# Performance work log

Measured on AMD Instinct MI355X. Metric: run time of the kernel, lower is better.

Reference implementation:

```python
import jax, jax.numpy as jnp
import numpy as np

N, E, F_IN, DIM, HEADS = 16384, 262144, 128, 64, 4
HID = DIM * HEADS  # 256
NEG = 0.2


def _lin(k, fan_in, fan_out):
    kw, kb = jax.random.split(k)
    s = 1.0 / np.sqrt(fan_in)
    return (jax.random.uniform(kw, (fan_in, fan_out), jnp.float32, -s, s),
            jax.random.uniform(kb, (fan_out,), jnp.float32, -s, s))


def setup_inputs() -> dict:
    key = jax.random.key(0)
    ks = jax.random.split(key, 20)
    x = jax.random.normal(ks[0], (N, F_IN), jnp.float32)
    edge_index = jax.random.randint(ks[1], (2, E), 0, N, jnp.int32)
    Win, b_in = _lin(ks[2], F_IN, DIM)
    Wskip, bskip = _lin(ks[3], DIM, HID)
    # conv1: in=DIM, out per head=DIM, heads=HEADS, concat -> HID
    Wl1, _ = _lin(ks[4], DIM, HID)
    Wr1, _ = _lin(ks[5], DIM, HID)
    att1 = jax.random.normal(ks[6], (HEADS, DIM), jnp.float32) * 0.1
    b1 = jnp.zeros((HID,), jnp.float32)
    # conv2: in=HID, out=HID, heads=1, concat=False
    Wl2, _ = _lin(ks[7], HID, HID)
    Wr2, _ = _lin(ks[8], HID, HID)
    att2 = jax.random.normal(ks[9], (1, HID), jnp.float32) * 0.1
    b2 = jnp.zeros((HID,), jnp.float32)
    # conv3: in=HID, out=HID, heads=1, concat=False
    Wl3, _ = _lin(ks[10], HID, HID)
    Wr3, _ = _lin(ks[11], HID, HID)
    att3 = jax.random.normal(ks[12], (1, HID), jnp.float32) * 0.1
    b3 = jnp.zeros((HID,), jnp.float32)
    Wm1, bm1 = _lin(ks[13], HID, DIM)
    Wm2, bm2 = _lin(ks[14], DIM, DIM)
    Wm3, bm3 = _lin(ks[15], DIM, 1)
    return dict(x=x, edge_index=edge_index, Win=Win, b_in=b_in,
                Wskip=Wskip, bskip=bskip,
                Wl1=Wl1, Wr1=Wr1, att1=att1, b1=b1,
                Wl2=Wl2, Wr2=Wr2, att2=att2, b2=b2,
                Wl3=Wl3, Wr3=Wr3, att3=att3, b3=b3,
                Wm1=Wm1, bm1=bm1, Wm2=Wm2, bm2=bm2, Wm3=Wm3, bm3=bm3)


def gatv2(x, src, dst, Wl, Wr, att, b, concat):
    # PyG GATv2Conv: x_l = lin_l(x)[src], x_r = lin_r(x)[dst]
    n = x.shape[0]
    H, D = att.shape
    xl = (x @ Wl).reshape(n, H, D)
    xr = (x @ Wr).reshape(n, H, D)
    e = jax.nn.leaky_relu(xl[src] + xr[dst], NEG)          # [E, H, D]
    logits = jnp.einsum('ehd,hd->eh', e, att)              # [E, H]
    m = jax.ops.segment_max(logits, dst, num_segments=n)   # per-dst softmax
    alpha = jnp.exp(logits - m[dst])
    denom = jax.ops.segment_sum(alpha, dst, num_segments=n)
    alpha = alpha / denom[dst]
    out = jax.ops.segment_sum(alpha[:, :, None] * xl[src], dst, num_segments=n)
    out = out.reshape(n, H * D) if concat else out.mean(axis=1)
    return out + b


def reference(x, edge_index, Win, b_in, Wskip, bskip,
              Wl1, Wr1, att1, b1, Wl2, Wr2, att2, b2,
              Wl3, Wr3, att3, b3, Wm1, bm1, Wm2, bm2, Wm3, bm3):
    n = x.shape[0]
    # add self loops (GATv2Conv default add_self_loops=True)
    loop = jnp.arange(n, dtype=edge_index.dtype)
    src = jnp.concatenate([edge_index[0], loop])
    dst = jnp.concatenate([edge_index[1], loop])

    h = jax.nn.relu(x @ Win + b_in)                         # [N, DIM]
    out1 = jax.nn.relu(gatv2(h, src, dst, Wl1, Wr1, att1, b1, True))
    out1 = out1 + (h @ Wskip + bskip)                       # [N, HID]
    out2 = jax.nn.relu(gatv2(out1, src, dst, Wl2, Wr2, att2, b2, False))
    out2 = out2 + out1
    out3 = jax.nn.relu(gatv2(out2, src, dst, Wl3, Wr3, att3, b3, False))
    out3 = out3 + out2
    out = jax.nn.relu(out3 @ Wm1 + bm1)
    out = jax.nn.relu(out @ Wm2 + bm2)
    out = out @ Wm3 + bm3                                   # [N, 1]
    return out.reshape(-1)
```

## Files before the change

kernel.cpp:

```cpp
#include <hip/hip_runtime.h>
#include <cstdint>
#include <cstddef>

#define N_NODES 16384
#define E_EDGES 262144
#define FIN     128
#define DIM     64
#define HID     256
#define NEG     0.2f

typedef _Float16 h8 __attribute__((ext_vector_type(8)));
typedef _Float16 h4 __attribute__((ext_vector_type(4)));
typedef _Float16 h2 __attribute__((ext_vector_type(2)));
typedef float    f32x4 __attribute__((ext_vector_type(4)));
typedef float    f32x2 __attribute__((ext_vector_type(2)));

__device__ __forceinline__ void csr_scan_body(const int* __restrict__ cnt,
                                              int* __restrict__ offs,
                                              int* __restrict__ cursor, int tid) {
    __shared__ int wsum[4];
    int lane = tid & 63, w = tid >> 6;
    int base = tid * 64;
    const int4* c4 = (const int4*)(cnt + base);
    int4 v[16];
    int s = 0;
#pragma unroll
    for (int i = 0; i < 16; ++i) {
        v[i] = c4[i];
        s += v[i].x + v[i].y + v[i].z + v[i].w;
    }
    int scan = s;
#pragma unroll
    for (int off = 1; off < 64; off <<= 1) {
        int t = __shfl_up(scan, off);
        if (lane >= off) scan += t;
    }
    if (lane == 63) wsum[w] = scan;
    __syncthreads();
    int wbase = 0;
#pragma unroll
    for (int i = 0; i < 4; ++i) if (i < w) wbase += wsum[i];
    int run = wbase + (scan - s);
#pragma unroll
    for (int i = 0; i < 16; ++i) {
        int4 o;
        o.x = run;
        o.y = o.x + v[i].x;
        o.z = o.y + v[i].y;
        o.w = o.z + v[i].z;
        *(int4*)(offs + base + 4 * i) = o;
        *(int4*)(cursor + base + 4 * i) = o;
        run = o.w + v[i].w;
    }
    if (tid == 255) offs[N_NODES] = run;
}

template<int K, bool RELU, bool O16, bool IN32>
__device__ __forceinline__ void mfma_n64_body(const void* __restrict__ Av,
                                              const _Float16* __restrict__ Wp,
                                              const float* __restrict__ bias,
                                              void* __restrict__ outv,
                                              int rowBase, int lane) {
    int l15 = lane & 15, l4 = lane >> 4;
    f32x4 acc[4][4] = {};
#pragma unroll
    for (int ks = 0; ks < K / 32; ++ks) {
        h8 af[4], bf[4];
#pragma unroll
        for (int mi = 0; mi < 4; ++mi) {
            if constexpr (IN32) {
                const float* ap = (const float*)Av + (size_t)(rowBase + mi * 16 + l15) * K + ks * 32 + l4 * 8;
                float4 a0 = *(const float4*)ap;
                float4 a1 = *(const float4*)(ap + 4);
                h8 v;
                v[0] = (_Float16)a0.x; v[1] = (_Float16)a0.y;
                v[2] = (_Float16)a0.z; v[3] = (_Float16)a0.w;
                v[4] = (_Float16)a1.x; v[5] = (_Float16)a1.y;
                v[6] = (_Float16)a1.z; v[7] = (_Float16)a1.w;
                af[mi] = v;
            } else {
                af[mi] = *(const h8*)((const _Float16*)Av + (size_t)(rowBase + mi * 16 + l15) * K + ks * 32 + l4 * 8);
            }
        }
#pragma unroll
        for (int ni = 0; ni < 4; ++ni)
            bf[ni] = *(const h8*)(Wp + ((size_t)(ks * 4 + l4) * 64 + ni * 16 + l15) * 8);
#pragma unroll
        for (int mi = 0; mi < 4; ++mi)
#pragma unroll
            for (int ni = 0; ni < 4; ++ni)
                acc[mi][ni] = __builtin_amdgcn_mfma_f32_16x16x32_f16(af[mi], bf[ni], acc[mi][ni], 0, 0, 0);
    }
#pragma unroll
    for (int mi = 0; mi < 4; ++mi)
#pragma unroll
        for (int ni = 0; ni < 4; ++ni) {
            int c = ni * 16 + l15;
            float bv = bias[c];
#pragma unroll
            for (int q = 0; q < 4; ++q) {
                int r = rowBase + mi * 16 + l4 * 4 + q;
                float v = acc[mi][ni][q] + bv;
                if (RELU) v = fmaxf(v, 0.f);
                if constexpr (O16) ((_Float16*)outv)[(size_t)r * 64 + c] = (_Float16)v;
                else               ((float*)outv)[(size_t)r * 64 + c] = v;
            }
        }
}

template<int K>
__device__ __forceinline__ void mfma_gemm_body(const _Float16* __restrict__ A,
                                               const _Float16* __restrict__ Wp,
                                               int NT,
                                               _Float16* __restrict__ o16a,
                                               _Float16* __restrict__ o16b,
                                               float* __restrict__ o32,
                                               const float* __restrict__ bias,
                                               int bx, int by, int tid) {
    int lane = tid & 63, wid = tid >> 6;
    int wm = wid >> 1, wn = wid & 1;
    int rowBase = bx * 128 + wm * 64;
    int colBase = by * 128 + wn * 64;
    int l15 = lane & 15, l4 = lane >> 4;

    f32x4 acc[4][4] = {};
#pragma unroll
    for (int ks = 0; ks < K / 32; ++ks) {
        h8 af[4], bf[4];
#pragma unroll
        for (int mi = 0; mi < 4; ++mi)
            af[mi] = *(const h8*)(A + (size_t)(rowBase + mi * 16 + l15) * K + ks * 32 + l4 * 8);
#pragma unroll
        for (int ni = 0; ni < 4; ++ni)
            bf[ni] = *(const h8*)(Wp + ((size_t)(ks * 4 + l4) * NT + colBase + ni * 16 + l15) * 8);
#pragma unroll
        for (int mi = 0; mi < 4; ++mi)
#pragma unroll
            for (int ni = 0; ni < 4; ++ni)
                acc[mi][ni] = __builtin_amdgcn_mfma_f32_16x16x32_f16(af[mi], bf[ni], acc[mi][ni], 0, 0, 0);
    }

    int seg = colBase >> 8;
    int cbase = colBase & 255;
    if (o32 != nullptr && seg == 2) {
#pragma unroll
        for (int mi = 0; mi < 4; ++mi)
#pragma unroll
            for (int ni = 0; ni < 4; ++ni) {
                int c = cbase + ni * 16 + l15;
                float bv = bias[c];
#pragma unroll
                for (int q = 0; q < 4; ++q) {
                    int r = rowBase + mi * 16 + l4 * 4 + q;
                    o32[(size_t)r * 256 + c] = acc[mi][ni][q] + bv;
                }
            }
    } else {
        _Float16* o = (seg == 0) ? o16a : o16b;
#pragma unroll
        for (int mi = 0; mi < 4; ++mi)
#pragma unroll
            for (int ni = 0; ni < 4; ++ni) {
                int c = cbase + ni * 16 + l15;
#pragma unroll
                for (int q = 0; q < 4; ++q) {
                    int r = rowBase + mi * 16 + l4 * 4 + q;
                    o[(size_t)r * 256 + c] = (_Float16)acc[mi][ni][q];
                }
            }
    }
}

struct PackJob { const float* W; _Float16* dst; int Ksrc, Nsrc, NT, colOff; };
struct PackJobs { PackJob j[10]; };

__global__ __launch_bounds__(256) void pack_all_kernel(PackJobs jobs, int* __restrict__ cnt) {
    int i = blockIdx.x * 256 + threadIdx.x;
    if (blockIdx.y == 10) {
        if (i < N_NODES) cnt[i] = 0;
        return;
    }
    PackJob jb = jobs.j[blockIdx.y];
    if (i < jb.Ksrc * jb.Nsrc) {
        int k = i / jb.Nsrc, n = i % jb.Nsrc;
        jb.dst[((size_t)(k >> 3) * jb.NT + jb.colOff + n) * 8 + (k & 7)] = (_Float16)jb.W[i];
    }
}

__global__ __launch_bounds__(256) void hist_inproj_kernel(const int* __restrict__ dst,
                                                          int* __restrict__ cnt,
                                                          const float* __restrict__ x,
                                                          const _Float16* __restrict__ Winp,
                                                          const float* __restrict__ b_in,
                                                          _Float16* __restrict__ h16) {
    int bx = blockIdx.x;
    if (bx < E_EDGES / 256) {
        int i = bx * 256 + threadIdx.x;
        atomicAdd(&cnt[dst[i]], 1);
        return;
    }
    int tid = threadIdx.x;
    int wid = tid >> 6, lane = tid & 63;
    int rowBase = (bx - E_EDGES / 256) * 256 + wid * 64;
    mfma_n64_body<FIN, true, true, true>(x, Winp, b_in, h16, rowBase, lane);
}

__global__ __launch_bounds__(256) void conv1_scan_kernel(const _Float16* __restrict__ A,
                                                         const _Float16* __restrict__ Wp,
                                                         _Float16* __restrict__ xl16,
                                                         _Float16* __restrict__ xr16,
                                                         float* __restrict__ skip,
                                                         const float* __restrict__ bskip,
                                                         const int* __restrict__ cnt,
                                                         int* __restrict__ offs,
                                                         int* __restrict__ cursor) {
    if (blockIdx.y == 6) {
        if (blockIdx.x == 0) csr_scan_body(cnt, offs, cursor, threadIdx.x);
        return;
    }
    mfma_gemm_body<64>(A, Wp, 768, xl16, xr16, skip, bskip, blockIdx.x, blockIdx.y, threadIdx.x);
}

__global__ __launch_bounds__(256) void scatter_kernel(const int* __restrict__ src,
                                                      const int* __restrict__ dst,
                                                      int* __restrict__ cursor,
                                                      int* __restrict__ esrc) {
    int i = blockIdx.x * 256 + threadIdx.x;
    if (i < E_EDGES) {
        int p = atomicAdd(&cursor[dst[i]], 1);
        esrc[p] = src[i];
    }
}

template<int K>
__global__ __launch_bounds__(256) void mfma_gemm_kernel(const _Float16* __restrict__ A,
                                                        const _Float16* __restrict__ Wp,
                                                        int NT,
                                                        _Float16* __restrict__ o16a,
                                                        _Float16* __restrict__ o16b,
                                                        float* __restrict__ o32,
                                                        const float* __restrict__ bias) {
    mfma_gemm_body<K>(A, Wp, NT, o16a, o16b, o32, bias, blockIdx.x, blockIdx.y, threadIdx.x);
}

template<int H, int OMODE>
__global__ __launch_bounds__(256) void gat_agg_kernel(const _Float16* __restrict__ xl,
                                                      const _Float16* __restrict__ xr,
                                                      const float* __restrict__ att,
                                                      const float* __restrict__ bias,
                                                      const float* __restrict__ resid,
                                                      const int* __restrict__ offs,
                                                      const int* __restrict__ esrc,
                                                      float* __restrict__ out,
                                                      _Float16* __restrict__ out16) {
    int tid = threadIdx.x;
    int wid = tid >> 6;
    int lane = tid & 63;
    int node = blockIdx.x * 4 + wid;
    int g  = lane >> 4;
    int li = lane & 15;

    h2 xrv[8];
    {
        const h8* xp = (const h8*)(xr + ((size_t)node << 8) + (li << 4));
        h8 a0 = __builtin_nontemporal_load(xp);
        h8 a1 = __builtin_nontemporal_load(xp + 1);
#pragma unroll
        for (int i = 0; i < 4; ++i) { xrv[i][0] = a0[2 * i]; xrv[i][1] = a0[2 * i + 1]; }
#pragma unroll
        for (int i = 0; i < 4; ++i) { xrv[4 + i][0] = a1[2 * i]; xrv[4 + i][1] = a1[2 * i + 1]; }
    }
    h2 attv[8];
    {
        const float4* ap = (const float4*)(att + (li << 4));
#pragma unroll
        for (int i = 0; i < 4; ++i) {
            float4 a = ap[i];
            attv[2 * i][0] = (_Float16)a.x; attv[2 * i][1] = (_Float16)a.y;
            attv[2 * i + 1][0] = (_Float16)a.z; attv[2 * i + 1][1] = (_Float16)a.w;
        }
    }
    const h2 negc = { (_Float16)NEG, (_Float16)NEG };

    int dbase = (li << 4) + (g << 2);
    float4 bv = *(const float4*)(bias + dbase);
    f32x4 rv = __builtin_nontemporal_load((const f32x4*)(resid + ((size_t)node << 8) + dbase));

    float m = -1e30f, s = 0.f;
    f32x2 acc2[8];
#pragma unroll
    for (int i = 0; i < 8; ++i) acc2[i] = (f32x2){0.f, 0.f};

    int e0 = offs[node];
    int total = offs[node + 1] - e0 + 1;

    auto gather = [&](int srcn, h2* hv) {
        const h8* xp = (const h8*)(xl + ((size_t)srcn << 8) + (li << 4));
        h8 a0 = xp[0], a1 = xp[1];
#pragma unroll
        for (int i = 0; i < 4; ++i) { hv[i][0] = a0[2 * i]; hv[i][1] = a0[2 * i + 1]; }
#pragma unroll
        for (int i = 0; i < 4; ++i) { hv[4 + i][0] = a1[2 * i]; hv[4 + i][1] = a1[2 * i + 1]; }
    };
    auto logit = [&](const h2* hv) -> float {
        float p0 = 0.f, p1 = 0.f;
#pragma unroll
        for (int i = 0; i < 4; ++i) {
            h2 sum = hv[i] + xrv[i];
            h2 lr = __builtin_elementwise_max(sum, sum * negc);
            p0 = __builtin_amdgcn_fdot2(lr, attv[i], p0, false);
            h2 sum2 = hv[4 + i] + xrv[4 + i];
            h2 lr2 = __builtin_elementwise_max(sum2, sum2 * negc);
            p1 = __builtin_amdgcn_fdot2(lr2, attv[4 + i], p1, false);
        }
        float part = p0 + p1;
        part += __shfl_xor(part, 1);
        part += __shfl_xor(part, 2);
        if constexpr (H == 1) {
            part += __shfl_xor(part, 4);
            part += __shfl_xor(part, 8);
        }
        return part;
    };

    int vi = g;
    int sA = 0, sB = 0;
    if (vi + 4 < total) {
        sA = (vi == 0) ? node : esrc[e0 + vi - 1];
        sB = esrc[e0 + vi + 3];
    }
    for (; vi + 4 < total; vi += 8) {
        int nvi = vi + 8;
        int ia = e0 + nvi - 1; if (ia > E_EDGES - 1) ia = E_EDGES - 1;
        int ib = e0 + nvi + 3; if (ib > E_EDGES - 1) ib = E_EDGES - 1;
        int sA2 = esrc[ia];
        int sB2 = esrc[ib];

        h2 hA[8], hB[8];
        gather(sA, hA);
        gather(sB, hB);
        float lpA = logit(hA);
        float lpB = logit(hB);
        float mx = fmaxf(lpA, lpB);
        if (mx > m + 8.f) {
            float c  = __expf(m - mx);
            float pA = __expf(lpA - mx);
            float pB = __expf(lpB - mx);
            s = s * c + pA + pB;
#pragma unroll
            for (int i = 0; i < 8; ++i) {
                f32x2 t = acc2[i] * c;
                t[0] = fmaf(pA, (float)hA[i][0], t[0]);
                t[1] = fmaf(pA, (float)hA[i][1], t[1]);
                t[0] = fmaf(pB, (float)hB[i][0], t[0]);
                t[1] = fmaf(pB, (float)hB[i][1], t[1]);
                acc2[i] = t;
            }
            m = mx;
        } else {
            float pA = __expf(lpA - m);
            float pB = __expf(lpB - m);
            s += pA + pB;
#pragma unroll
            for (int i = 0; i < 8; ++i) {
                f32x2 t = acc2[i];
                t[0] = fmaf(pA, (float)hA[i][0], t[0]);
                t[1] = fmaf(pA, (float)hA[i][1], t[1]);
                t[0] = fmaf(pB, (float)hB[i][0], t[0]);
                t[1] = fmaf(pB, (float)hB[i][1], t[1]);
                acc2[i] = t;
            }
        }
        sA = sA2; sB = sB2;
    }
    for (; vi < total; vi += 4) {
        int srcn = (vi == 0) ? node : esrc[e0 + vi - 1];
        h2 hA[8];
        gather(srcn, hA);
        float lp = logit(hA);
        if (lp > m + 8.f) {
            float c = __expf(m - lp);
            s = s * c + 1.f;
#pragma unroll
            for (int i = 0; i < 8; ++i) {
                f32x2 t = acc2[i] * c;
                t[0] = t[0] + (float)hA[i][0];
                t[1] = t[1] + (float)hA[i][1];
                acc2[i] = t;
            }
            m = lp;
        } else {
            float p = __expf(lp - m);
            s += p;
#pragma unroll
            for (int i = 0; i < 8; ++i) {
                f32x2 t = acc2[i];
                t[0] = fmaf(p, (float)hA[i][0], t[0]);
                t[1] = fmaf(p, (float)hA[i][1], t[1]);
                acc2[i] = t;
            }
        }
    }

#pragma unroll
    for (int mask = 16; mask <= 32; mask <<= 1) {
        float m2 = __shfl_xor(m, mask);
        float s2 = __shfl_xor(s, mask);
        float M = fmaxf(m, m2);
        float c1 = __expf(m - M);
        float c2 = __expf(m2 - M);
        s = s * c1 + s2 * c2;
#pragma unroll
        for (int i = 0; i < 8; ++i) {
            float ax = __shfl_xor(acc2[i][0], mask);
            float ay = __shfl_xor(acc2[i][1], mask);
            acc2[i][0] = acc2[i][0] * c1 + ax * c2;
            acc2[i][1] = acc2[i][1] * c1 + ay * c2;
        }
        m = M;
    }

    float inv = 1.f / s;
    float a0, a1v, a2, a3;
    if (g == 0)      { a0 = acc2[0][0]; a1v = acc2[0][1]; a2 = acc2[1][0]; a3 = acc2[1][1]; }
    else if (g == 1) { a0 = acc2[2][0]; a1v = acc2[2][1]; a2 = acc2[3][0]; a3 = acc2[3][1]; }
    else if (g == 2) { a0 = acc2[4][0]; a1v = acc2[4][1]; a2 = acc2[5][0]; a3 = acc2[5][1]; }
    else             { a0 = acc2[6][0]; a1v = acc2[6][1]; a2 = acc2[7][0]; a3 = acc2[7][1]; }
    float o0 = fmaxf(a0 * inv + bv.x, 0.f) + rv[0];
    float o1 = fmaxf(a1v * inv + bv.y, 0.f) + rv[1];
    float o2 = fmaxf(a2 * inv + bv.z, 0.f) + rv[2];
    float o3 = fmaxf(a3 * inv + bv.w, 0.f) + rv[3];
    if constexpr (OMODE != 2) {
        float4 ov = make_float4(o0, o1, o2, o3);
        *(float4*)(out + ((size_t)node << 8) + dbase) = ov;
    }
    if constexpr (OMODE != 0) {
        h4 hv;
        hv[0] = (_Float16)o0; hv[1] = (_Float16)o1;
        hv[2] = (_Float16)o2; hv[3] = (_Float16)o3;
        *(h4*)(out16 + ((size_t)node << 8) + dbase) = hv;
    }
}

__global__ __launch_bounds__(256) void mlp_head_kernel(const _Float16* __restrict__ A,
                                                       const _Float16* __restrict__ Wm1p,
                                                       const float* __restrict__ bm1,
                                                       const _Float16* __restrict__ Wm2p,
                                                       const float* __restrict__ bm2,
                                                       const float* __restrict__ Wm3,
                                                       const float* __restrict__ bm3,
                                                       float* __restrict__ out) {
    __shared__ _Float16 t1s[4][16][72];
    int tid = threadIdx.x;
    int lane = tid & 63, wid = tid >> 6;
    int rowBase = blockIdx.x * 64 + wid * 16;
    int l15 = lane & 15, l4 = lane >> 4;

    f32x4 acc[4] = {};
#pragma unroll
    for (int ks = 0; ks < 8; ++ks) {
        h8 af = __builtin_nontemporal_load((const h8*)(A + (size_t)(rowBase + l15) * 256 + ks * 32 + l4 * 8));
        h8 bf[4];
#pragma unroll
        for (int ni = 0; ni < 4; ++ni)
            bf[ni] = *(const h8*)(Wm1p + ((size_t)(ks * 4 + l4) * 64 + ni * 16 + l15) * 8);
#pragma unroll
        for (int ni = 0; ni < 4; ++ni)
            acc[ni] = __builtin_amdgcn_mfma_f32_16x16x32_f16(af, bf[ni], acc[ni], 0, 0, 0);
    }
#pragma unroll
    for (int ni = 0; ni < 4; ++ni) {
        int c = ni * 16 + l15;
        float bv = bm1[c];
#pragma unroll
        for (int q = 0; q < 4; ++q)
            t1s[wid][l4 * 4 + q][c] = (_Float16)fmaxf(acc[ni][q] + bv, 0.f);
    }

    f32x4 acc2[4] = {};
#pragma unroll
    for (int ks = 0; ks < 2; ++ks) {
        h8 af = *(const h8*)&t1s[wid][l15][ks * 32 + l4 * 8];
        h8 bf[4];
#pragma unroll
        for (int ni = 0; ni < 4; ++ni)
            bf[ni] = *(const h8*)(Wm2p + ((size_t)(ks * 4 + l4) * 64 + ni * 16 + l15) * 8);
#pragma unroll
        for (int ni = 0; ni < 4; ++ni)
            acc2[ni] = __builtin_amdgcn_mfma_f32_16x16x32_f16(af, bf[ni], acc2[ni], 0, 0, 0);
    }

    float b3 = bm3[0];
    float b2v[4], w3v[4];
#pragma unroll
    for (int ni = 0; ni < 4; ++ni) {
        b2v[ni] = bm2[ni * 16 + l15];
        w3v[ni] = Wm3[ni * 16 + l15];
    }
#pragma unroll
    for (int q = 0; q < 4; ++q) {
        float part = 0.f;
#pragma unroll
        for (int ni = 0; ni < 4; ++ni)
            part += fmaxf(acc2[ni][q] + b2v[ni], 0.f) * w3v[ni];
        part += __shfl_xor(part, 1);
        part += __shfl_xor(part, 2);
        part += __shfl_xor(part, 4);
        part += __shfl_xor(part, 8);
        if (l15 == 0)
            out[rowBase + l4 * 4 + q] = part + b3;
    }
}

extern "C" void kernel_launch(void* const* d_in, const int* in_sizes, int n_in,
                              void* d_out, int out_size, void* d_ws, size_t ws_size,
                              hipStream_t stream) {
    const float* x     = (const float*)d_in[0];
    const int*   ei    = (const int*)d_in[1];
    const float* Win   = (const float*)d_in[2];
    const float* b_in  = (const float*)d_in[3];
    const float* Wskip = (const float*)d_in[4];
    const float* bskip = (const float*)d_in[5];
    const float* Wl1   = (const float*)d_in[6];
    const float* Wr1   = (const float*)d_in[7];
    const float* att1  = (const float*)d_in[8];
    const float* b1    = (const float*)d_in[9];
    const float* Wl2   = (const float*)d_in[10];
    const float* Wr2   = (const float*)d_in[11];
    const float* att2  = (const float*)d_in[12];
    const float* b2    = (const float*)d_in[13];
    const float* Wl3   = (const float*)d_in[14];
    const float* Wr3   = (const float*)d_in[15];
    const float* att3  = (const float*)d_in[16];
    const float* b3    = (const float*)d_in[17];
    const float* Wm1   = (const float*)d_in[18];
    const float* bm1   = (const float*)d_in[19];
    const float* Wm2   = (const float*)d_in[20];
    const float* bm2   = (const float*)d_in[21];
    const float* Wm3   = (const float*)d_in[22];
    const float* bm3   = (const float*)d_in[23];

    char* p = (char*)d_ws;
    auto alloc = [&](size_t bytes) { char* r = p; p += (bytes + 255) & ~(size_t)255; return r; };
    const size_t NN = N_NODES;
    float*    skip = (float*)alloc(NN * 256 * 4);
    float*    out1 = (float*)alloc(NN * 256 * 4);
    _Float16* o116 = (_Float16*)alloc(NN * 256 * 2);
    _Float16* o216 = (_Float16*)alloc(NN * 256 * 2);
    _Float16* o316 = o116;
    _Float16* h16  = (_Float16*)alloc(NN * 64 * 2);
    _Float16* xl16 = (_Float16*)alloc(NN * 256 * 2);
    _Float16* xr16 = (_Float16*)alloc(NN * 256 * 2);
    _Float16* Wp1  = (_Float16*)alloc((size_t)64 * 768 * 2);
    _Float16* Wp2  = (_Float16*)alloc((size_t)256 * 512 * 2);
    _Float16* Wp3  = (_Float16*)alloc((size_t)256 * 512 * 2);
    _Float16* Winp = (_Float16*)alloc((size_t)128 * 64 * 2);
    _Float16* Wm1p = (_Float16*)alloc((size_t)256 * 64 * 2);
    _Float16* Wm2p = (_Float16*)alloc((size_t)64 * 64 * 2);
    int* cnt    = (int*)alloc(N_NODES * 4);
    int* offs   = (int*)alloc((N_NODES + 1) * 4);
    int* cursor = (int*)alloc(N_NODES * 4);
    int* esrc   = (int*)alloc(E_EDGES * 4);

    const int* src = ei;
    const int* dst = ei + E_EDGES;

    PackJobs jobs = {{
        { Wl1,   Wp1,  64,  256, 768, 0   },
        { Wr1,   Wp1,  64,  256, 768, 256 },
        { Wskip, Wp1,  64,  256, 768, 512 },
        { Wl2,   Wp2,  256, 256, 512, 0   },
        { Wr2,   Wp2,  256, 256, 512, 256 },
        { Wl3,   Wp3,  256, 256, 512, 0   },
        { Wr3,   Wp3,  256, 256, 512, 256 },
        { Win,   Winp, 128, 64,  64,  0   },
        { Wm1,   Wm1p, 256, 64,  64,  0   },
        { Wm2,   Wm2p, 64,  64,  64,  0   },
    }};
    pack_all_kernel<<<dim3(256, 11), 256, 0, stream>>>(jobs, cnt);

    hist_inproj_kernel<<<E_EDGES / 256 + N_NODES / 256, 256, 0, stream>>>(
        dst, cnt, x, Winp, b_in, h16);

    conv1_scan_kernel<<<dim3(128, 7), 256, 0, stream>>>(
        h16, Wp1, xl16, xr16, skip, bskip, cnt, offs, cursor);

    scatter_kernel<<<E_EDGES / 256, 256, 0, stream>>>(src, dst, cursor, esrc);

    gat_agg_kernel<4, 1><<<N_NODES / 4, 256, 0, stream>>>(xl16, xr16, att1, b1, skip, offs, esrc, out1, o116);

    mfma_gemm_kernel<256><<<dim3(128, 4), 256, 0, stream>>>(o116, Wp2, 512, xl16, xr16, nullptr, nullptr);
    gat_agg_kernel<1, 1><<<N_NODES / 4, 256, 0, stream>>>(xl16, xr16, att2, b2, out1, offs, esrc, skip , o216);

    mfma_gemm_kernel<256><<<dim3(128, 4), 256, 0, stream>>>(o216, Wp3, 512, xl16, xr16, nullptr, nullptr);
    gat_agg_kernel<1, 2><<<N_NODES / 4, 256, 0, stream>>>(xl16, xr16, att3, b3, skip , offs, esrc, nullptr, o316);

    mlp_head_kernel<<<N_NODES / 64, 256, 0, stream>>>(o316, Wm1p, bm1, Wm2p, bm2, Wm3, bm3, (float*)d_out);
}
```

Baseline: 194.8 us.

## Split conv1 aggregation into two half-width passes over head pairs

Replaces the single 4-head conv1 aggregation kernel with a new kernel launched twice. Each launch handles 128 of the 256 feature columns (two heads). Each 16-lane group covers one half row, and the four groups in a wavefront process different edges in parallel before merging their online-softmax state with shuffles. The aim is to shrink the per-pass gather footprint so it sits better in cache and to add edge-level parallelism per node. The cost is that the edge list and offsets are read twice and there is an extra launch.

```diff
diff --git a/kernel.cpp b/kernel.cpp
--- a/kernel.cpp
+++ b/kernel.cpp
@@ -241,6 +241,194 @@
                                                         float* __restrict__ o32,
                                                         const float* __restrict__ bias) {
     mfma_gemm_body<K>(A, Wp, NT, o16a, o16b, o32, bias, blockIdx.x, blockIdx.y, threadIdx.x);
+}
+
+template<int OMODE>
+__global__ __launch_bounds__(256) void gat_agg_half_kernel(const _Float16* __restrict__ xl,
+                                                           const _Float16* __restrict__ xr,
+                                                           const float* __restrict__ att,
+                                                           const float* __restrict__ bias,
+                                                           const float* __restrict__ resid,
+                                                           const int* __restrict__ offs,
+                                                           const int* __restrict__ esrc,
+                                                           float* __restrict__ out,
+                                                           _Float16* __restrict__ out16,
+                                                           int halfOff) {
+    int tid = threadIdx.x;
+    int wid = tid >> 6;
+    int lane = tid & 63;
+    int node = blockIdx.x * 4 + wid;
+    int g  = lane >> 4;
+    int li = lane & 15;
+    int dlane = halfOff + (li << 3);
+
+    h2 xrv[4];
+    {
+        h8 a0 = *(const h8*)(xr + ((size_t)node << 8) + dlane);
+#pragma unroll
+        for (int i = 0; i < 4; ++i) { xrv[i][0] = a0[2 * i]; xrv[i][1] = a0[2 * i + 1]; }
+    }
+    h2 attv[4];
+    {
+        const float4* ap = (const float4*)(att + dlane);
+        float4 a = ap[0], b = ap[1];
+        attv[0][0] = (_Float16)a.x; attv[0][1] = (_Float16)a.y;
+        attv[1][0] = (_Float16)a.z; attv[1][1] = (_Float16)a.w;
+        attv[2][0] = (_Float16)b.x; attv[2][1] = (_Float16)b.y;
+        attv[3][0] = (_Float16)b.z; attv[3][1] = (_Float16)b.w;
+    }
+    const h2 negc = { (_Float16)NEG, (_Float16)NEG };
+
+    int dbase = dlane + (g << 1);
+    float bv0 = bias[dbase], bv1 = bias[dbase + 1];
+    float rv0 = resid[((size_t)node << 8) + dbase];
+    float rv1 = resid[((size_t)node << 8) + dbase + 1];
+
+    float m = -1e30f, s = 0.f;
+    f32x2 acc2[4];
+#pragma unroll
+    for (int i = 0; i < 4; ++i) acc2[i] = (f32x2){0.f, 0.f};
+
+    int e0 = offs[node];
+    int total = offs[node + 1] - e0 + 1;
+
+    auto gather = [&](int srcn, h2* hv) {
+        h8 a0 = *(const h8*)(xl + ((size_t)srcn << 8) + dlane);
+#pragma unroll
+        for (int i = 0; i < 4; ++i) { hv[i][0] = a0[2 * i]; hv[i][1] = a0[2 * i + 1]; }
+    };
+    auto logit = [&](const h2* hv) -> float {
+        float p0 = 0.f, p1 = 0.f;
+#pragma unroll
+        for (int i = 0; i < 2; ++i) {
+            h2 sum = hv[i] + xrv[i];
+            h2 lr = __builtin_elementwise_max(sum, sum * negc);
+            p0 = __builtin_amdgcn_fdot2(lr, attv[i], p0, false);
+            h2 sum2 = hv[2 + i] + xrv[2 + i];
+            h2 lr2 = __builtin_elementwise_max(sum2, sum2 * negc);
+            p1 = __builtin_amdgcn_fdot2(lr2, attv[2 + i], p1, false);
+        }
+        float part = p0 + p1;
+        part += __shfl_xor(part, 1);
+        part += __shfl_xor(part, 2);
+        part += __shfl_xor(part, 4);
+        return part;
+    };
+
+    int vi = g;
+    int sA = 0, sB = 0;
+    if (vi + 4 < total) {
+        sA = (vi == 0) ? node : esrc[e0 + vi - 1];
+        sB = esrc[e0 + vi + 3];
+    }
+    for (; vi + 4 < total; vi += 8) {
+        int nvi = vi + 8;
+        int ia = e0 + nvi - 1; if (ia > E_EDGES - 1) ia = E_EDGES - 1;
+        int ib = e0 + nvi + 3; if (ib > E_EDGES - 1) ib = E_EDGES - 1;
+        int sA2 = esrc[ia];
+        int sB2 = esrc[ib];
+
+        h2 hA[4], hB[4];
+        gather(sA, hA);
+        gather(sB, hB);
+        float lpA = logit(hA);
+        float lpB = logit(hB);
+        float mx = fmaxf(lpA, lpB);
+        if (mx > m + 8.f) {
+            float c  = __expf(m - mx);
+            float pA = __expf(lpA - mx);
+            float pB = __expf(lpB - mx);
+            s = s * c + pA + pB;
+#pragma unroll
+            for (int i = 0; i < 4; ++i) {
+                f32x2 t = acc2[i] * c;
+                t[0] = fmaf(pA, (float)hA[i][0], t[0]);
+                t[1] = fmaf(pA, (float)hA[i][1], t[1]);
+                t[0] = fmaf(pB, (float)hB[i][0], t[0]);
+                t[1] = fmaf(pB, (float)hB[i][1], t[1]);
+                acc2[i] = t;
+            }
+            m = mx;
+        } else {
+            float pA = __expf(lpA - m);
+            float pB = __expf(lpB - m);
+            s += pA + pB;
+#pragma unroll
+            for (int i = 0; i < 4; ++i) {
+                f32x2 t = acc2[i];
+                t[0] = fmaf(pA, (float)hA[i][0], t[0]);
+                t[1] = fmaf(pA, (float)hA[i][1], t[1]);
+                t[0] = fmaf(pB, (float)hB[i][0], t[0]);
+                t[1] = fmaf(pB, (float)hB[i][1], t[1]);
+                acc2[i] = t;
+            }
+        }
+        sA = sA2; sB = sB2;
+    }
+    for (; vi < total; vi += 4) {
+        int srcn = (vi == 0) ? node : esrc[e0 + vi - 1];
+        h2 hA[4];
+        gather(srcn, hA);
+        float lp = logit(hA);
+        if (lp > m + 8.f) {
+            float c = __expf(m - lp);
+            s = s * c + 1.f;
+#pragma unroll
+            for (int i = 0; i < 4; ++i) {
+                f32x2 t = acc2[i] * c;
+                t[0] = t[0] + (float)hA[i][0];
+                t[1] = t[1] + (float)hA[i][1];
+                acc2[i] = t;
+            }
+            m = lp;
+        } else {
+            float p = __expf(lp - m);
+            s += p;
+#pragma unroll
+            for (int i = 0; i < 4; ++i) {
+                f32x2 t = acc2[i];
+                t[0] = fmaf(p, (float)hA[i][0], t[0]);
+                t[1] = fmaf(p, (float)hA[i][1], t[1]);
+                acc2[i] = t;
+            }
+        }
+    }
+
+#pragma unroll
+    for (int mask = 16; mask <= 32; mask <<= 1) {
+        float m2 = __shfl_xor(m, mask);
+        float s2 = __shfl_xor(s, mask);
+        float M = fmaxf(m, m2);
+        float c1 = __expf(m - M);
+        float c2 = __expf(m2 - M);
+        s = s * c1 + s2 * c2;
+#pragma unroll
+        for (int i = 0; i < 4; ++i) {
+            float ax = __shfl_xor(acc2[i][0], mask);
+            float ay = __shfl_xor(acc2[i][1], mask);
+            acc2[i][0] = acc2[i][0] * c1 + ax * c2;
+            acc2[i][1] = acc2[i][1] * c1 + ay * c2;
+        }
+        m = M;
+    }
+
+    float inv = 1.f / s;
+    float a0, a1v;
+    if (g == 0)      { a0 = acc2[0][0]; a1v = acc2[0][1]; }
+    else if (g == 1) { a0 = acc2[1][0]; a1v = acc2[1][1]; }
+    else if (g == 2) { a0 = acc2[2][0]; a1v = acc2[2][1]; }
+    else             { a0 = acc2[3][0]; a1v = acc2[3][1]; }
+    float o0 = fmaxf(a0 * inv + bv0, 0.f) + rv0;
+    float o1 = fmaxf(a1v * inv + bv1, 0.f) + rv1;
+    if constexpr (OMODE != 2) {
+        f32x2 ov = { o0, o1 };
+        *(f32x2*)(out + ((size_t)node << 8) + dbase) = ov;
+    }
+    if constexpr (OMODE != 0) {
+        h2 hv;
+        hv[0] = (_Float16)o0; hv[1] = (_Float16)o1;
+        *(h2*)(out16 + ((size_t)node << 8) + dbase) = hv;
+    }
 }
 
 template<int H, int OMODE>
@@ -587,7 +775,10 @@
 
     scatter_kernel<<<E_EDGES / 256, 256, 0, stream>>>(src, dst, cursor, esrc);
 
-    gat_agg_kernel<4, 1><<<N_NODES / 4, 256, 0, stream>>>(xl16, xr16, att1, b1, skip, offs, esrc, out1, o116);
+    gat_agg_half_kernel<1><<<N_NODES / 4, 256, 0, stream>>>(
+        xl16, xr16, att1, b1, skip, offs, esrc, out1, o116, 0);
+    gat_agg_half_kernel<1><<<N_NODES / 4, 256, 0, stream>>>(
+        xl16, xr16, att1, b1, skip, offs, esrc, out1, o116, 128);
 
     mfma_gemm_kernel<256><<<dim3(128, 4), 256, 0, stream>>>(o116, Wp2, 512, xl16, xr16, nullptr, nullptr);
     gat_agg_kernel<1, 1><<<N_NODES / 4, 256, 0, stream>>>(xl16, xr16, att2, b2, out1, offs, esrc, skip , o216);
```

Measured after the change: 199.2 us. 2.3% more time.
